# Kernel optimization log

Hardware: AMD Instinct MI355X
Metric: run time of the kernel (lower is better)

## Reference

```python
import jax, jax.numpy as jnp
import numpy as np

NUM_HEADS = 4
INITIAL_VALUE = 1.0
HEADS_RANGE = 3.0


def rotate_every_two(x):
    x1 = x[..., ::2]
    x2 = x[..., 1::2]
    return jnp.stack([-x2, x1], axis=-1).reshape(x.shape)


def theta_shift(x, sin, cos):
    return x * cos + rotate_every_two(x) * sin


def rel_pos_2d(h, w, key_dim):
    # angle: repeat each frequency twice -> length key_dim
    base = 1.0 / 10000.0 ** jnp.linspace(0.0, 1.0, key_dim // 2)
    angle = jnp.repeat(base, 2)
    decay = jnp.log(1.0 - 2.0 ** (-(INITIAL_VALUE + HEADS_RANGE * jnp.arange(NUM_HEADS, dtype=jnp.float32) / NUM_HEADS)))
    idx = jnp.arange(h * w, dtype=jnp.float32)
    sin = jnp.sin(idx[:, None] * angle[None, :]).reshape(h, w, key_dim)
    cos = jnp.cos(idx[:, None] * angle[None, :]).reshape(h, w, key_dim)
    def decay_1d(l):
        i = jnp.arange(l, dtype=jnp.float32)
        return jnp.abs(i[:, None] - i[None, :])[None, :, :] * decay[:, None, None]  # (n, l, l)
    return sin, cos, decay_1d(h), decay_1d(w)


def setup_inputs() -> dict:
    key = jax.random.key(0)
    b, C, H, W = 16, 256, 64, 64
    ks = jax.random.split(key, 12)
    gain = 2.0 ** (-2.5)
    xav = (2.0 / (C + C)) ** 0.5
    return {
        "x": jax.random.normal(ks[0], (b, C, H, W), jnp.float32),
        "Wq": jax.random.normal(ks[1], (C, C), jnp.float32) * gain * xav,
        "bq": jnp.zeros((C,), jnp.float32),
        "Wk": jax.random.normal(ks[2], (C, C), jnp.float32) * gain * xav,
        "bk": jnp.zeros((C,), jnp.float32),
        "Wv": jax.random.normal(ks[3], (C, C), jnp.float32) * gain * xav,
        "bv": jnp.zeros((C,), jnp.float32),
        "dw_kernel": jax.random.normal(ks[4], (5, 5, 1, C), jnp.float32) * 0.05,
        "dw_bias": jnp.zeros((C,), jnp.float32),
        "Wo": jax.random.normal(ks[5], (C, C), jnp.float32) * xav,
        "bo": jnp.zeros((C,), jnp.float32),
    }


def reference(x, Wq, bq, Wk, bk, Wv, bv, dw_kernel, dw_bias, Wo, bo):
    x = jnp.transpose(x, (0, 2, 3, 1))  # (b, h, w, c)
    b, h, w, c = x.shape
    n = NUM_HEADS
    d = c // n  # key_dim == head_dim (value_factor=1)
    scaling = d ** (-0.5)

    sin, cos, mask_h, mask_w = rel_pos_2d(h, w, d)

    q = x @ Wq + bq
    k = (x @ Wk + bk) * scaling
    v = x @ Wv + bv  # (b, h, w, c)

    # depthwise 5x5 conv (lepe) on v, NHWC
    lepe = jax.lax.conv_general_dilated(
        v, dw_kernel, window_strides=(1, 1), padding=((2, 2), (2, 2)),
        dimension_numbers=("NHWC", "HWIO", "NHWC"), feature_group_count=c,
    ) + dw_bias

    q = q.reshape(b, h, w, n, d).transpose(0, 3, 1, 2, 4)  # (b, n, h, w, d)
    k = k.reshape(b, h, w, n, d).transpose(0, 3, 1, 2, 4)
    qr = theta_shift(q, sin, cos)  # sin/cos (h,w,d) broadcast
    kr = theta_shift(k, sin, cos)

    # width-axis attention: rows independent
    qr_w = qr.transpose(0, 2, 1, 3, 4)  # (b, h, n, w, d)
    kr_w = kr.transpose(0, 2, 1, 3, 4)
    v5 = v.reshape(b, h, w, n, d).transpose(0, 1, 3, 2, 4)  # (b, h, n, w, d)
    qk_w = jnp.einsum("bhnqd,bhnkd->bhnqk", qr_w, kr_w) + mask_w  # (b,h,n,w,w)
    v5 = jnp.einsum("bhnqk,bhnkd->bhnqd", jax.nn.softmax(qk_w, axis=-1), v5)

    # height-axis attention: columns independent
    qr_h = qr.transpose(0, 3, 1, 2, 4)  # (b, w, n, h, d)
    kr_h = kr.transpose(0, 3, 1, 2, 4)
    v6 = v5.transpose(0, 3, 2, 1, 4)  # (b, w, n, h, d)
    qk_h = jnp.einsum("bwnqd,bwnkd->bwnqk", qr_h, kr_h) + mask_h  # (b,w,n,h,h)
    out = jnp.einsum("bwnqk,bwnkd->bwnqd", jax.nn.softmax(qk_h, axis=-1), v6)

    out = out.transpose(0, 3, 1, 2, 4).reshape(b, h, w, c)  # (b,h,w,n*d)
    out = (out + lepe) @ Wo + bo
    return jnp.transpose(out, (0, 3, 1, 2))  # (b, c, h, w)
```

## Files before the change

### kernel.cpp

```cpp
#include <hip/hip_runtime.h>
#include <hip/hip_bf16.h>

typedef unsigned short u16;
typedef unsigned int   u32;
typedef __attribute__((ext_vector_type(8))) short bf16x8;
typedef __attribute__((ext_vector_type(4))) float f32x4;

__device__ __forceinline__ float bf2f(u16 u) {
    union { u32 i; float f; } x; x.i = ((u32)u) << 16; return x.f;
}
__device__ __forceinline__ u16 f2bf(float f) {
    union { float f; u32 i; } x; x.f = f;
    u32 i = x.i;
    u32 r = (i + 0x7fffu + ((i >> 16) & 1u)) >> 16;
    return (u16)r;
}

__global__ void k_tables(float2* __restrict__ csT) {
    int id = blockIdx.x * 256 + threadIdx.x;
    int t = id >> 5, i = id & 31;
    double ang = pow(10000.0, -(double)i / 31.0);
    double a = (double)t * ang;
    csT[id] = make_float2((float)cos(a), (float)sin(a));
}

__global__ __launch_bounds__(256) void k_prep_w(
    const float* __restrict__ Wq, const float* __restrict__ Wk,
    const float* __restrict__ Wv, const float* __restrict__ Wo,
    u16* __restrict__ WTq, u16* __restrict__ WTk,
    u16* __restrict__ WTv, u16* __restrict__ WoT)
{
    __shared__ float T[32][33];
    int z = blockIdx.z;
    const float* W = (z == 0) ? Wq : (z == 1) ? Wk : (z == 2) ? Wv : Wo;
    u16* WT        = (z == 0) ? WTq : (z == 1) ? WTk : (z == 2) ? WTv : WoT;
    int n0 = blockIdx.x * 32, k0 = blockIdx.y * 32;
    int tx = threadIdx.x & 31, ty = threadIdx.x >> 5;
#pragma unroll
    for (int i = 0; i < 4; i++)
        T[ty * 4 + i][tx] = W[(k0 + ty * 4 + i) * 256 + n0 + tx];
    __syncthreads();
#pragma unroll
    for (int i = 0; i < 4; i++)
        WT[(n0 + ty * 4 + i) * 256 + k0 + tx] = f2bf(T[tx][ty * 4 + i]);
}

__global__ __launch_bounds__(256) void k_prep_x(
    const float* __restrict__ x, u16* __restrict__ xT)
{
    __shared__ float T[32][33];
    int b = blockIdx.z, c0 = blockIdx.y * 32, s0 = blockIdx.x * 32;
    int tx = threadIdx.x & 31, ty = threadIdx.x >> 5;
#pragma unroll
    for (int i = 0; i < 4; i++)
        T[ty * 4 + i][tx] = x[((size_t)(b * 256 + c0 + ty * 4 + i)) * 4096 + s0 + tx];
    __syncthreads();
#pragma unroll
    for (int i = 0; i < 4; i++)
        xT[((size_t)(b * 4096 + s0 + ty * 4 + i)) * 256 + c0 + tx] = f2bf(T[tx][ty * 4 + i]);
}

__global__ __launch_bounds__(512, 1) void k_qkv_fused(
    const u16* __restrict__ xT, const u16* __restrict__ WTall,
    const float* __restrict__ bq, const float* __restrict__ bk,
    const float* __restrict__ bv,
    const float2* __restrict__ csT,
    u16* __restrict__ qr, u16* __restrict__ kr, u16* __restrict__ vO)
{
    __shared__ alignas(16) u16 Alds[128 * 256];
    __shared__ alignas(16) u16 Blds[2][256 * 64];
    __shared__ float2 SL[128 * 32];

    const int tid = threadIdx.x;
    const int t0 = blockIdx.x * 128;
    const int ar = tid >> 5, ac = tid & 31;
    const int br = tid >> 3, bc = tid & 7;

    bf16x8 breg[4];
    {
        bf16x8 areg[8];
#pragma unroll
        for (int p = 0; p < 8; ++p)
            areg[p] = *(const bf16x8*)(xT + (size_t)(t0 + p * 16 + ar) * 256 + ac * 8);
#pragma unroll
        for (int p = 0; p < 4; ++p)
            breg[p] = *(const bf16x8*)(WTall + (size_t)(p * 64 + br) * 256 + bc * 8);
#pragma unroll
        for (int p = 0; p < 8; ++p) {
            int r = p * 16 + ar;
            *(bf16x8*)(Alds + r * 256 + (ac ^ (r & 7)) * 8) = areg[p];
        }
        const int sb = t0 & 4095;
#pragma unroll
        for (int p = 0; p < 8; ++p) {
            int idx = p * 512 + tid;
            SL[idx] = csT[(size_t)sb * 32 + idx];
        }
    }

    const int lane = tid & 63, w = tid >> 6;
    const int wr = w >> 2, wc = w & 3;
    const int l15 = lane & 15, l4 = lane >> 4, l7 = lane & 7;

#pragma unroll
    for (int mat = 0; mat < 3; ++mat) {
        f32x4 acc[4][4];
#pragma unroll
        for (int mi = 0; mi < 4; ++mi)
#pragma unroll
            for (int ni = 0; ni < 4; ++ni) acc[mi][ni] = (f32x4)0.f;

#pragma unroll
        for (int ks = 0; ks < 4; ++ks) {
            const int s = mat * 4 + ks;
            u16* Bl = &Blds[s & 1][0];
#pragma unroll
            for (int p = 0; p < 4; ++p) {
                int r = p * 64 + br;
                *(bf16x8*)(Bl + r * 64 + (bc ^ (r & 7)) * 8) = breg[p];
            }
            __syncthreads();
            if (s < 11) {
                const int s2 = s + 1;
                const int mat2 = s2 >> 2, ks2 = s2 & 3;
#pragma unroll
                for (int p = 0; p < 4; ++p)
                    breg[p] = *(const bf16x8*)(WTall + (size_t)mat2 * 65536 +
                                (size_t)(p * 64 + br) * 256 + ks2 * 64 + bc * 8);
            }
#pragma unroll
            for (int kk = 0; kk < 2; ++kk) {
                bf16x8 af[4], bfr[4];
#pragma unroll
                for (int mi = 0; mi < 4; ++mi) {
                    int r = wr * 64 + mi * 16 + l15;
                    af[mi] = *(const bf16x8*)(Alds + r * 256 + (ks * 8 + ((kk * 4 + l4) ^ l7)) * 8);
                }
#pragma unroll
                for (int ni = 0; ni < 4; ++ni) {
                    int r = wc * 64 + ni * 16 + l15;
                    bfr[ni] = *(const bf16x8*)(Bl + r * 64 + ((kk * 4 + l4) ^ l7) * 8);
                }
#pragma unroll
                for (int mi = 0; mi < 4; ++mi)
#pragma unroll
                    for (int ni = 0; ni < 4; ++ni)
                        acc[mi][ni] = __builtin_amdgcn_mfma_f32_16x16x32_bf16(
                            af[mi], bfr[ni], acc[mi][ni], 0, 0, 0);
            }
        }

        const float* bias = (mat == 0) ? bq : (mat == 1) ? bk : bv;
        u16* out          = (mat == 0) ? qr : (mat == 1) ? kr : vO;
        const float kscale = (mat == 1) ? 0.125f : 1.0f;
        float bcol[4]; int ip[4];
#pragma unroll
        for (int ni = 0; ni < 4; ++ni) {
            bcol[ni] = bias[wc * 64 + ni * 16 + l15];
            ip[ni] = (ni * 16 + l15) >> 1;
        }
#pragma unroll
        for (int mi = 0; mi < 4; ++mi) {
#pragma unroll
            for (int rg = 0; rg < 4; ++rg) {
                const int sl = wr * 64 + mi * 16 + l4 * 4 + rg;
                size_t trow = (size_t)(t0 + sl) * 256;
#pragma unroll
                for (int ni = 0; ni < 4; ++ni) {
                    float val = acc[mi][ni][rg] + bcol[ni];
                    float res;
                    if (mat != 2) {
                        val *= kscale;
                        float prt = __shfl_xor(val, 1);
                        float2 cs = SL[sl * 32 + ip[ni]];
                        res = (lane & 1) ? fmaf(val, cs.x,  prt * cs.y)
                                         : fmaf(val, cs.x, -prt * cs.y);
                    } else {
                        res = val;
                    }
                    float res2 = __shfl_xor(res, 1);
                    if (!(lane & 1)) {
                        u32 pk;
                        asm("v_cvt_pk_bf16_f32 %0, %1, %2" : "=v"(pk) : "v"(res), "v"(res2));
                        int o = wc * 64 + ni * 16 + l15;
                        *(u32*)(out + trow + o) = pk;
                    }
                }
            }
        }
    }
}

__global__ __launch_bounds__(256) void k_lepe(
    const u16* __restrict__ v, const float* __restrict__ dwk,
    const float* __restrict__ dwb, u16* __restrict__ lepe)
{
    __shared__ u16 VhU[12 * 12 * 64];
    __shared__ float Kl[25][64];
    const int b = blockIdx.z, cg = blockIdx.y * 64;
    const int ty0 = (blockIdx.x >> 3) * 8, tx0 = (blockIdx.x & 7) * 8;
    const int tid = threadIdx.x;

    for (int idx = tid; idx < 1600; idx += 256) {
        int tap = idx >> 6, c = idx & 63;
        Kl[tap][c] = dwk[tap * 256 + cg + c];
    }
#pragma unroll
    for (int p = 0; p < 9; ++p) {
        int idx = p * 256 + tid;
        int ch = idx & 15, pos = idx >> 4;
        int py = pos / 12, px = pos - py * 12;
        int gy = ty0 + py - 2, gx = tx0 + px - 2;
        ushort4 val = make_ushort4(0, 0, 0, 0);
        if (gy >= 0 && gy < 64 && gx >= 0 && gx < 64)
            val = *(const ushort4*)(v + (size_t)(b * 4096 + gy * 64 + gx) * 256 + cg + ch * 4);
        *(ushort4*)(VhU + pos * 64 + ch * 4) = val;
    }
    __syncthreads();

    const int c = tid & 63, pg = tid >> 6;
    float kreg[25];
#pragma unroll
    for (int t = 0; t < 25; t++) kreg[t] = Kl[t][c];
    const float bias = dwb[cg + c];

    float acc[2][8];
#pragma unroll
    for (int t = 0; t < 2; ++t)
#pragma unroll
        for (int ox = 0; ox < 8; ++ox) acc[t][ox] = bias;

#pragma unroll
    for (int rr = 0; rr < 6; ++rr) {
        const int r = pg * 2 + rr;
        float rv[12];
#pragma unroll
        for (int px = 0; px < 12; ++px)
            rv[px] = bf2f(VhU[(r * 12 + px) * 64 + c]);
        if (rr <= 4) {
            const int dy = rr;
#pragma unroll
            for (int ox = 0; ox < 8; ++ox)
#pragma unroll
                for (int dx = 0; dx < 5; ++dx)
                    acc[0][ox] = fmaf(rv[ox + dx], kreg[dy * 5 + dx], acc[0][ox]);
        }
        if (rr >= 1) {
            const int dy = rr - 1;
#pragma unroll
            for (int ox = 0; ox < 8; ++ox)
#pragma unroll
                for (int dx = 0; dx < 5; ++dx)
                    acc[1][ox] = fmaf(rv[ox + dx], kreg[dy * 5 + dx], acc[1][ox]);
        }
    }

#pragma unroll
    for (int t = 0; t < 2; ++t) {
        const int oy = pg * 2 + t;
#pragma unroll
        for (int ox = 0; ox < 8; ++ox)
            lepe[(size_t)(b * 4096 + (ty0 + oy) * 64 + tx0 + ox) * 256 + cg + c] =
                f2bf(acc[t][ox]);
    }
}

template <int AXIS>
__global__ __launch_bounds__(256) void k_attn_mfma(
    const u16* __restrict__ qr, const u16* __restrict__ kr,
    const u16* __restrict__ vsrc, const u16* __restrict__ lepeP,
    u16* __restrict__ outb)
{
    __shared__ u16 VT[4][64 * 72];
    __shared__ u16 PL[4][64 * 72];

    const int tid = threadIdx.x;
    const int w = tid >> 6, lane = tid & 63;
    const int l15 = lane & 15, l4 = lane >> 4;
    const int wid = blockIdx.x * 4 + w;
    const int b = wid >> 8, xy = (wid >> 2) & 63, n = wid & 3;

    size_t qkbase, vbase; int qkstride, vstride;
    if (AXIS == 0) {
        qkbase = ((size_t)(b * 4096 + xy * 64)) * 256 + n * 64;
        qkstride = 256;
        vbase = qkbase; vstride = 256;
    } else {
        qkbase = ((size_t)(b * 4096 + xy)) * 256 + n * 64;
        qkstride = 64 * 256;
        vbase = ((size_t)((b * 64 + xy) * 4 + n)) * 4096;
        vstride = 64;
    }

    u16* VTl = &VT[w][0];
    u16* PLl = &PL[w][0];

    bf16x8 vld[8];
    const int vrow = lane >> 3, vchunk = lane & 7;
#pragma unroll
    for (int it = 0; it < 8; ++it)
        vld[it] = *(const bf16x8*)(vsrc + vbase + (size_t)(it * 8 + vrow) * vstride + vchunk * 8);

    bf16x8 ka[4][2], qb[4][2];
#pragma unroll
    for (int t = 0; t < 4; ++t)
#pragma unroll
        for (int ks = 0; ks < 2; ++ks) {
            ka[t][ks] = *(const bf16x8*)(kr + qkbase + (size_t)(t * 16 + l15) * qkstride + ks * 32 + l4 * 8);
            qb[t][ks] = *(const bf16x8*)(qr + qkbase + (size_t)(t * 16 + l15) * qkstride + ks * 32 + l4 * 8);
        }

    f32x4 sacc[4][4];
#pragma unroll
    for (int kt = 0; kt < 4; ++kt)
#pragma unroll
        for (int qt = 0; qt < 4; ++qt) sacc[kt][qt] = (f32x4)0.f;
#pragma unroll
    for (int ks = 0; ks < 2; ++ks)
#pragma unroll
        for (int kt = 0; kt < 4; ++kt)
#pragma unroll
            for (int qt = 0; qt < 4; ++qt)
                sacc[kt][qt] = __builtin_amdgcn_mfma_f32_16x16x32_bf16(
                    ka[kt][ks], qb[qt][ks], sacc[kt][qt], 0, 0, 0);

#pragma unroll
    for (int it = 0; it < 8; ++it) {
        int gp = ((it ^ vchunk) << 3) + vrow;
#pragma unroll
        for (int j = 0; j < 8; ++j) {
            int d = vchunk * 8 + j;
            VTl[d * 72 + gp] = (u16)vld[it][j];
        }
    }

    const float decay = logf(1.0f - exp2f(-(1.0f + 0.75f * (float)n)));
#pragma unroll
    for (int qt = 0; qt < 4; ++qt) {
        const int qq = qt * 16 + l15;
        float lsum = 0.f;
#pragma unroll
        for (int kt = 0; kt < 4; ++kt) {
            const int kb = kt * 16 + l4 * 4;
#pragma unroll
            for (int rr = 0; rr < 4; ++rr) {
                float s = sacc[kt][qt][rr] + fabsf((float)(qq - kb - rr)) * decay;
                s = __expf(s);
                sacc[kt][qt][rr] = s;
                lsum += s;
            }
        }
        lsum += __shfl_xor(lsum, 16);
        lsum += __shfl_xor(lsum, 32);
        const float rinv = 1.0f / lsum;
#pragma unroll
        for (int kt = 0; kt < 4; ++kt) {
            float e0 = sacc[kt][qt][0] * rinv, e1 = sacc[kt][qt][1] * rinv;
            float e2 = sacc[kt][qt][2] * rinv, e3 = sacc[kt][qt][3] * rinv;
            u32 p0, p1;
            asm("v_cvt_pk_bf16_f32 %0, %1, %2" : "=v"(p0) : "v"(e0), "v"(e1));
            asm("v_cvt_pk_bf16_f32 %0, %1, %2" : "=v"(p1) : "v"(e2), "v"(e3));
            uint2 pp; pp.x = p0; pp.y = p1;
            *(uint2*)(PLl + (qt * 16 + l15) * 72 + kt * 16 + l4 * 4) = pp;
        }
    }

    __builtin_amdgcn_s_waitcnt(0xC07F);
    bf16x8 pa[4][2], vb[4][2];
#pragma unroll
    for (int qt = 0; qt < 4; ++qt)
#pragma unroll
        for (int ks = 0; ks < 2; ++ks)
            pa[qt][ks] = *(const bf16x8*)(PLl + (qt * 16 + l15) * 72 + ks * 32 + l4 * 8);
#pragma unroll
    for (int dt = 0; dt < 4; ++dt)
#pragma unroll
        for (int ks = 0; ks < 2; ++ks) {
            int d = dt * 16 + l15;
            int g = (ks * 4 + l4) ^ (d >> 3);
            vb[dt][ks] = *(const bf16x8*)(VTl + d * 72 + g * 8);
        }

    f32x4 oacc[4][4];
#pragma unroll
    for (int qt = 0; qt < 4; ++qt)
#pragma unroll
        for (int dt = 0; dt < 4; ++dt) oacc[qt][dt] = (f32x4)0.f;
#pragma unroll
    for (int ks = 0; ks < 2; ++ks)
#pragma unroll
        for (int qt = 0; qt < 4; ++qt)
#pragma unroll
            for (int dt = 0; dt < 4; ++dt)
                oacc[qt][dt] = __builtin_amdgcn_mfma_f32_16x16x32_bf16(
                    pa[qt][ks], vb[dt][ks], oacc[qt][dt], 0, 0, 0);

#pragma unroll
    for (int qt = 0; qt < 4; ++qt)
#pragma unroll
        for (int dt = 0; dt < 4; ++dt)
#pragma unroll
            for (int rr = 0; rr < 4; ++rr)
                PLl[(qt * 16 + l4 * 4 + rr) * 72 + dt * 16 + l15] = f2bf(oacc[qt][dt][rr]);
    __builtin_amdgcn_s_waitcnt(0xC07F);

    size_t orow;
    if (AXIS == 0) orow = ((size_t)((b * 64 + lane) * 4 + n)) * 4096 + xy * 64;
    else           orow = ((size_t)(b * 4096 + lane * 64 + xy)) * 256 + n * 64;
#pragma unroll
    for (int c = 0; c < 8; ++c) {
        bf16x8 o8 = *(const bf16x8*)(PLl + lane * 72 + c * 8);
        if (AXIS == 1) {
            bf16x8 lp = *(const bf16x8*)(lepeP + orow + c * 8);
            u16 hv[8];
#pragma unroll
            for (int j = 0; j < 8; ++j)
                hv[j] = f2bf(bf2f((u16)o8[j]) + bf2f((u16)lp[j]));
            o8 = *(bf16x8*)hv;
        }
        *(bf16x8*)(outb + orow + c * 8) = o8;
    }
}

__global__ __launch_bounds__(512, 1) void k_proj_fused(
    const u16* __restrict__ WoT, const u16* __restrict__ attnL,
    const float* __restrict__ bo, float* __restrict__ y)
{
    __shared__ alignas(16) u16 Alds[128 * 256];
    __shared__ alignas(16) u16 Blds[2][256 * 64];

    const int tid = threadIdx.x;
    const int bid = blockIdx.x;
    const int xcd = bid & 7, slot = bid >> 3;
    const int tt = xcd * 32 + (slot >> 1);
    const int oh = slot & 1;
    const int t0 = tt * 256;
    const int o0 = oh * 128;

    const int ar = tid >> 5, ac = tid & 31;
    const int br = tid >> 3, bc = tid & 7;

    bf16x8 breg[4];
    {
        bf16x8 areg[8];
#pragma unroll
        for (int p = 0; p < 8; ++p)
            areg[p] = *(const bf16x8*)(WoT + (size_t)(o0 + p * 16 + ar) * 256 + ac * 8);
#pragma unroll
        for (int p = 0; p < 4; ++p)
            breg[p] = *(const bf16x8*)(attnL + (size_t)(t0 + p * 64 + br) * 256 + bc * 8);
#pragma unroll
        for (int p = 0; p < 8; ++p) {
            int r = p * 16 + ar;
            *(bf16x8*)(Alds + r * 256 + (ac ^ (r & 7)) * 8) = areg[p];
        }
    }

    const int lane = tid & 63, w = tid >> 6;
    const int wr = w >> 2, wc = w & 3;
    const int l15 = lane & 15, l4 = lane >> 4, l7 = lane & 7;

    f32x4 acc[4][4];
#pragma unroll
    for (int mi = 0; mi < 4; ++mi)
#pragma unroll
        for (int ni = 0; ni < 4; ++ni) acc[mi][ni] = (f32x4)0.f;

#pragma unroll
    for (int ks = 0; ks < 4; ++ks) {
        u16* Bl = &Blds[ks & 1][0];
#pragma unroll
        for (int p = 0; p < 4; ++p) {
            int r = p * 64 + br;
            *(bf16x8*)(Bl + r * 64 + (bc ^ (r & 7)) * 8) = breg[p];
        }
        __syncthreads();
        if (ks < 3) {
#pragma unroll
            for (int p = 0; p < 4; ++p)
                breg[p] = *(const bf16x8*)(attnL + (size_t)(t0 + p * 64 + br) * 256 + (ks + 1) * 64 + bc * 8);
        }
#pragma unroll
        for (int kk = 0; kk < 2; ++kk) {
            bf16x8 af[4], bfr[4];
#pragma unroll
            for (int mi = 0; mi < 4; ++mi) {
                int r = wr * 64 + mi * 16 + l15;
                af[mi] = *(const bf16x8*)(Alds + r * 256 + (ks * 8 + ((kk * 4 + l4) ^ l7)) * 8);
            }
#pragma unroll
            for (int ni = 0; ni < 4; ++ni) {
                int r = wc * 64 + ni * 16 + l15;
                bfr[ni] = *(const bf16x8*)(Bl + r * 64 + ((kk * 4 + l4) ^ l7) * 8);
            }
#pragma unroll
            for (int mi = 0; mi < 4; ++mi)
#pragma unroll
                for (int ni = 0; ni < 4; ++ni)
                    acc[mi][ni] = __builtin_amdgcn_mfma_f32_16x16x32_bf16(
                        af[mi], bfr[ni], acc[mi][ni], 0, 0, 0);
        }
    }

    const int b = t0 >> 12, sb = t0 & 4095;
#pragma unroll
    for (int mi = 0; mi < 4; ++mi) {
#pragma unroll
        for (int rg = 0; rg < 4; ++rg) {
            int o = o0 + wr * 64 + mi * 16 + l4 * 4 + rg;
            float bb = bo[o];
            float* yrow = y + ((size_t)(b * 256 + o)) * 4096 + sb + wc * 64;
#pragma unroll
            for (int ni = 0; ni < 4; ++ni)
                yrow[ni * 16 + l15] = acc[mi][ni][rg] + bb;
        }
    }
}

extern "C" void kernel_launch(void* const* d_in, const int* in_sizes, int n_in,
                              void* d_out, int out_size, void* d_ws, size_t ws_size,
                              hipStream_t stream)
{
    const float* x   = (const float*)d_in[0];
    const float* Wq  = (const float*)d_in[1];
    const float* bq  = (const float*)d_in[2];
    const float* Wk  = (const float*)d_in[3];
    const float* bk  = (const float*)d_in[4];
    const float* Wv  = (const float*)d_in[5];
    const float* bv  = (const float*)d_in[6];
    const float* dwk = (const float*)d_in[7];
    const float* dwb = (const float*)d_in[8];
    const float* Wo  = (const float*)d_in[9];
    const float* bo  = (const float*)d_in[10];
    float* y = (float*)d_out;

    char* ws = (char*)d_ws;
    const size_t MB = 1024 * 1024;
    float2* csT = (float2*)(ws);
    u16* WTq = (u16*)(ws + 1 * MB);
    u16* WTk = WTq + 65536;
    u16* WTv = WTk + 65536;
    u16* WoT = WTv + 65536;
    u16* qr   = (u16*)(ws + 2 * MB);
    u16* kr   = (u16*)(ws + 2 * MB + 32 * MB);
    u16* v    = (u16*)(ws + 2 * MB + 64 * MB);
    u16* lepe = (u16*)(ws + 2 * MB + 96 * MB);
    u16* xT   = (u16*)(ws + 2 * MB + 128 * MB);
    u16* v5   = xT;
    u16* attn = v;

    k_tables<<<dim3(512), dim3(256), 0, stream>>>(csT);
    k_prep_w<<<dim3(8, 8, 4), dim3(256), 0, stream>>>(Wq, Wk, Wv, Wo, WTq, WTk, WTv, WoT);
    k_prep_x<<<dim3(128, 8, 16), dim3(256), 0, stream>>>(x, xT);
    k_qkv_fused<<<dim3(512), dim3(512), 0, stream>>>(
        xT, WTq, bq, bk, bv, csT, qr, kr, v);
    k_lepe<<<dim3(64, 4, 16), dim3(256), 0, stream>>>(v, dwk, dwb, lepe);
    k_attn_mfma<0><<<dim3(1024), dim3(256), 0, stream>>>(qr, kr, v, nullptr, v5);
    k_attn_mfma<1><<<dim3(1024), dim3(256), 0, stream>>>(qr, kr, v5, lepe, attn);
    k_proj_fused<<<dim3(512), dim3(512), 0, stream>>>(WoT, attn, bo, y);
}
```

Before: 212.3 us.

## Fuse NCHW-to-token transpose and bf16 cast of x into QKV GEMM kernel

Removes the separate k_prep_x kernel and instead has k_qkv_fused read fp32 x directly in NCHW layout, staging it through the B-tile LDS buffer, transposing, converting to bf16 and writing it into the swizzled A tile. This avoids writing and re-reading a full bf16 xT intermediate in global memory plus one kernel launch. The rotary epilogue is also reworked to compute both outputs of each pair from a single shuffle instead of two. The cost is extra LDS traffic, two block-wide barriers, and serialized fp32 loads inside a kernel that runs one block per CU.

```diff
diff --git a/kernel.cpp b/kernel.cpp
--- a/kernel.cpp
+++ b/kernel.cpp
@@ -45,23 +45,8 @@
         WT[(n0 + ty * 4 + i) * 256 + k0 + tx] = f2bf(T[tx][ty * 4 + i]);
 }
 
-__global__ __launch_bounds__(256) void k_prep_x(
-    const float* __restrict__ x, u16* __restrict__ xT)
-{
-    __shared__ float T[32][33];
-    int b = blockIdx.z, c0 = blockIdx.y * 32, s0 = blockIdx.x * 32;
-    int tx = threadIdx.x & 31, ty = threadIdx.x >> 5;
-#pragma unroll
-    for (int i = 0; i < 4; i++)
-        T[ty * 4 + i][tx] = x[((size_t)(b * 256 + c0 + ty * 4 + i)) * 4096 + s0 + tx];
-    __syncthreads();
-#pragma unroll
-    for (int i = 0; i < 4; i++)
-        xT[((size_t)(b * 4096 + s0 + ty * 4 + i)) * 256 + c0 + tx] = f2bf(T[tx][ty * 4 + i]);
-}
-
 __global__ __launch_bounds__(512, 1) void k_qkv_fused(
-    const u16* __restrict__ xT, const u16* __restrict__ WTall,
+    const float* __restrict__ x, const u16* __restrict__ WTall,
     const float* __restrict__ bq, const float* __restrict__ bk,
     const float* __restrict__ bv,
     const float2* __restrict__ csT,
@@ -73,23 +58,44 @@
 
     const int tid = threadIdx.x;
     const int t0 = blockIdx.x * 128;
-    const int ar = tid >> 5, ac = tid & 31;
     const int br = tid >> 3, bc = tid & 7;
 
     bf16x8 breg[4];
+#pragma unroll
+    for (int p = 0; p < 4; ++p)
+        breg[p] = *(const bf16x8*)(WTall + (size_t)(p * 64 + br) * 256 + bc * 8);
+
     {
-        bf16x8 areg[8];
-#pragma unroll
-        for (int p = 0; p < 8; ++p)
-            areg[p] = *(const bf16x8*)(xT + (size_t)(t0 + p * 16 + ar) * 256 + ac * 8);
-#pragma unroll
-        for (int p = 0; p < 4; ++p)
-            breg[p] = *(const bf16x8*)(WTall + (size_t)(p * 64 + br) * 256 + bc * 8);
-#pragma unroll
-        for (int p = 0; p < 8; ++p) {
-            int r = p * 16 + ar;
-            *(bf16x8*)(Alds + r * 256 + (ac ^ (r & 7)) * 8) = areg[p];
-        }
+        float* Bf = (float*)&Blds[0][0];
+        const int b0 = t0 >> 12, sb0 = t0 & 4095;
+        const float* xb = x + ((size_t)b0 * 256) * 4096 + sb0;
+#pragma unroll
+        for (int ch = 0; ch < 2; ++ch) {
+#pragma unroll
+            for (int p = 0; p < 8; ++p) {
+                int it = p * 512 + tid;
+                int c = it >> 5, s4 = (it & 31) * 4;
+                float4 v4 = *(const float4*)(xb + (size_t)(ch * 128 + c) * 4096 + s4);
+                *(float4*)(Bf + c * 128 + s4) = v4;
+            }
+            __syncthreads();
+#pragma unroll
+            for (int p = 0; p < 4; ++p) {
+                int it = p * 512 + tid;
+                int tok = it & 127, ck = it >> 7;
+                u16 tmp[8];
+#pragma unroll
+                for (int j = 0; j < 8; ++j)
+                    tmp[j] = f2bf(Bf[(ck * 8 + j) * 128 + tok]);
+                int gc = ch * 16 + ck;
+                int gcs = (gc & 24) | ((gc & 7) ^ (tok & 7));
+                *(bf16x8*)(Alds + tok * 256 + gcs * 8) = *(bf16x8*)tmp;
+            }
+            __syncthreads();
+        }
+    }
+
+    {
         const int sb = t0 & 4095;
 #pragma unroll
         for (int p = 0; p < 8; ++p) {
@@ -167,18 +173,16 @@
                 size_t trow = (size_t)(t0 + sl) * 256;
 #pragma unroll
                 for (int ni = 0; ni < 4; ++ni) {
-                    float val = acc[mi][ni][rg] + bcol[ni];
-                    float res;
+                    float val = (acc[mi][ni][rg] + bcol[ni]) * kscale;
+                    float prt = __shfl_xor(val, 1);
+                    float res, res2;
                     if (mat != 2) {
-                        val *= kscale;
-                        float prt = __shfl_xor(val, 1);
                         float2 cs = SL[sl * 32 + ip[ni]];
-                        res = (lane & 1) ? fmaf(val, cs.x,  prt * cs.y)
-                                         : fmaf(val, cs.x, -prt * cs.y);
+                        res  = fmaf(val, cs.x, -prt * cs.y);
+                        res2 = fmaf(prt, cs.x,  val * cs.y);
                     } else {
-                        res = val;
+                        res = val; res2 = prt;
                     }
-                    float res2 = __shfl_xor(res, 1);
                     if (!(lane & 1)) {
                         u32 pk;
                         asm("v_cvt_pk_bf16_f32 %0, %1, %2" : "=v"(pk) : "v"(res), "v"(res2));
@@ -545,15 +549,13 @@
     u16* kr   = (u16*)(ws + 2 * MB + 32 * MB);
     u16* v    = (u16*)(ws + 2 * MB + 64 * MB);
     u16* lepe = (u16*)(ws + 2 * MB + 96 * MB);
-    u16* xT   = (u16*)(ws + 2 * MB + 128 * MB);
-    u16* v5   = xT;
+    u16* v5   = (u16*)(ws + 2 * MB + 128 * MB);
     u16* attn = v;
 
     k_tables<<<dim3(512), dim3(256), 0, stream>>>(csT);
     k_prep_w<<<dim3(8, 8, 4), dim3(256), 0, stream>>>(Wq, Wk, Wv, Wo, WTq, WTk, WTv, WoT);
-    k_prep_x<<<dim3(128, 8, 16), dim3(256), 0, stream>>>(x, xT);
     k_qkv_fused<<<dim3(512), dim3(512), 0, stream>>>(
-        xT, WTq, bq, bk, bv, csT, qr, kr, v);
+        x, WTq, bq, bk, bv, csT, qr, kr, v);
     k_lepe<<<dim3(64, 4, 16), dim3(256), 0, stream>>>(v, dwk, dwb, lepe);
     k_attn_mfma<0><<<dim3(1024), dim3(256), 0, stream>>>(qr, kr, v, nullptr, v5);
     k_attn_mfma<1><<<dim3(1024), dim3(256), 0, stream>>>(qr, kr, v5, lepe, attn);
```

New measurement: 196.8 us. 7.3% less time.
